# Optimization experiments

Hardware: AMD Instinct MI355X
Metric: run time of the kernel (lower is better)

Reference implementation:

```python
import jax, jax.numpy as jnp
import numpy as np

N, D, H = 2048, 128, 40


def setup_inputs() -> dict:
    key = jax.random.key(0)
    kx, kw, kv = jax.random.split(key, 3)
    X = jax.random.normal(kx, (N, D), dtype=jnp.float32)
    # nn.Parameter(torch.randn(D, D) / D) per head, stacked over H
    W = jax.random.normal(kw, (H, D, D), dtype=jnp.float32) / D
    V = jax.random.normal(kv, (H, D, D), dtype=jnp.float32) / D
    return {"X": X, "W": W, "V": V}


def reference(X, W, V):
    d = X.shape[1]
    # scores[h] = X @ W[h] @ X.T / sqrt(D)   -> [H, N, N]
    XW = jnp.einsum("nd,hde->hne", X, W)
    scores = jnp.einsum("hne,me->hnm", XW, X) / jnp.sqrt(jnp.asarray(d, X.dtype))
    # softmax over dim=1 of the 2D per-head score matrix == last axis here
    weights = jax.nn.softmax(scores, axis=-1) + 1e-8
    # A[h] = weights[h] @ X @ V[h]; output = sum over heads -> [N, D]
    XV = jnp.einsum("md,hde->hme", X, V)
    out = jnp.einsum("hnm,hme->ne", weights, XV)
    return out
```

## Files before the change

kernel.cpp:

```cpp
#include <hip/hip_runtime.h>
#include <hip/hip_bf16.h>
#include <stdint.h>

#define N 2048
#define D 128
#define H 40
#define NT 16

typedef __attribute__((ext_vector_type(8))) short short8;
typedef __attribute__((ext_vector_type(4))) float float4v;
typedef __attribute__((ext_vector_type(16))) float float16v;
typedef __attribute__((ext_vector_type(4))) _Float16 half4v;

static __device__ __forceinline__ unsigned short f32_to_bf16(float f) {
  unsigned int u = __builtin_bit_cast(unsigned int, f);
  unsigned int rounding = 0x7FFFu + ((u >> 16) & 1u);
  return (unsigned short)((u + rounding) >> 16);
}

static __device__ __forceinline__ unsigned int pk2(float lo, float hi) {
  return (unsigned int)f32_to_bf16(lo) | ((unsigned int)f32_to_bf16(hi) << 16);
}

static __device__ __forceinline__ unsigned int pk2f(float lo, float hi) {
  unsigned int a = __builtin_bit_cast(unsigned int, lo) + 0x8000u;
  unsigned int b = __builtin_bit_cast(unsigned int, hi) + 0x8000u;
  return __builtin_amdgcn_perm(b, a, 0x07060302u);
}

static __device__ __forceinline__ unsigned long long pack4(float x0, float x1,
                                                           float x2, float x3) {
  return (unsigned long long)pk2(x0, x1) | ((unsigned long long)pk2(x2, x3) << 32);
}

static __device__ __forceinline__ float fast_exp2(float x) {
#if __has_builtin(__builtin_amdgcn_exp2f)
  return __builtin_amdgcn_exp2f(x);
#else
  return __expf(0.69314718056f * x);
#endif
}

static __device__ __forceinline__ float bf2f(unsigned short u) {
  unsigned int x = ((unsigned int)u) << 16;
  return __builtin_bit_cast(float, x);
}

static __device__ __forceinline__ long long mk64(unsigned int lo, unsigned int hi) {
  return (long long)(((unsigned long long)hi << 32) | lo);
}

static __device__ __forceinline__ void load_lds16(const void* g, void* l) {
  __builtin_amdgcn_global_load_lds(
      (const __attribute__((address_space(1))) unsigned int*)g,
      (__attribute__((address_space(3))) unsigned int*)l, 16, 0, 0);
}

#define MFMA32(a, b, c) __builtin_amdgcn_mfma_f32_32x32x16_bf16((a), (b), (c), 0, 0, 0)
#define MFMA8(a, b, c) __builtin_amdgcn_mfma_f32_32x32x16_fp8_fp8((a), (b), (c), 0, 0, 0)

static __device__ __forceinline__ void regs_to_bfrags(const float16v c, int hh,
                                                      short8& f0, short8& f1) {
  unsigned int a0 = pk2f(c[0], c[1]),   a1 = pk2f(c[2], c[3]);
  unsigned int a2 = pk2f(c[4], c[5]),   a3 = pk2f(c[6], c[7]);
  unsigned int a4 = pk2f(c[8], c[9]),   a5 = pk2f(c[10], c[11]);
  unsigned int a6 = pk2f(c[12], c[13]), a7 = pk2f(c[14], c[15]);
  unsigned int x0 = __shfl_xor(hh ? a0 : a2, 32);
  unsigned int x1 = __shfl_xor(hh ? a1 : a3, 32);
  unsigned int x2 = __shfl_xor(hh ? a4 : a6, 32);
  unsigned int x3 = __shfl_xor(hh ? a5 : a7, 32);
  uint4 u0 = {hh ? x0 : a0, hh ? x1 : a1, hh ? a2 : x0, hh ? a3 : x1};
  uint4 u1 = {hh ? x2 : a4, hh ? x3 : a5, hh ? a6 : x2, hh ? a7 : x3};
  f0 = __builtin_bit_cast(short8, u0);
  f1 = __builtin_bit_cast(short8, u1);
}

static __device__ __forceinline__ void regs_to_f8frags(const float16v c, int hh,
                                                       long long& f0, long long& f1) {
  const float s = 64.0f;
  int v0 = __builtin_amdgcn_cvt_pk_fp8_f32(c[0] * s, c[1] * s, 0, false);
  v0 = __builtin_amdgcn_cvt_pk_fp8_f32(c[2] * s, c[3] * s, v0, true);
  int v1 = __builtin_amdgcn_cvt_pk_fp8_f32(c[4] * s, c[5] * s, 0, false);
  v1 = __builtin_amdgcn_cvt_pk_fp8_f32(c[6] * s, c[7] * s, v1, true);
  int v2 = __builtin_amdgcn_cvt_pk_fp8_f32(c[8] * s, c[9] * s, 0, false);
  v2 = __builtin_amdgcn_cvt_pk_fp8_f32(c[10] * s, c[11] * s, v2, true);
  int v3 = __builtin_amdgcn_cvt_pk_fp8_f32(c[12] * s, c[13] * s, 0, false);
  v3 = __builtin_amdgcn_cvt_pk_fp8_f32(c[14] * s, c[15] * s, v3, true);
  int t0 = __shfl_xor(hh ? v0 : v1, 32);
  int t1 = __shfl_xor(hh ? v2 : v3, 32);
  f0 = hh ? mk64((unsigned)t0, (unsigned)v1) : mk64((unsigned)v0, (unsigned)t0);
  f1 = hh ? mk64((unsigned)t1, (unsigned)v3) : mk64((unsigned)v2, (unsigned)t1);
}

static __device__ __forceinline__ void regs_to_pfrags(const float16v s, int hh,
                                                      float& lsum, short8& f0,
                                                      short8& f1) {
  float e[16];
  float acc = 0.0f;
#pragma unroll
  for (int i = 0; i < 16; i++) { e[i] = fast_exp2(s[i] * 0.015625f); acc += e[i]; }
  lsum += acc;
  unsigned int a0 = pk2f(e[0], e[1]),   a1 = pk2f(e[2], e[3]);
  unsigned int a2 = pk2f(e[4], e[5]),   a3 = pk2f(e[6], e[7]);
  unsigned int a4 = pk2f(e[8], e[9]),   a5 = pk2f(e[10], e[11]);
  unsigned int a6 = pk2f(e[12], e[13]), a7 = pk2f(e[14], e[15]);
  unsigned int x0 = __shfl_xor(hh ? a0 : a2, 32);
  unsigned int x1 = __shfl_xor(hh ? a1 : a3, 32);
  unsigned int x2 = __shfl_xor(hh ? a4 : a6, 32);
  unsigned int x3 = __shfl_xor(hh ? a5 : a7, 32);
  uint4 u0 = {hh ? x0 : a0, hh ? x1 : a1, hh ? a2 : x0, hh ? a3 : x1};
  uint4 u1 = {hh ? x2 : a4, hh ? x3 : a5, hh ? a6 : x2, hh ? a7 : x3};
  f0 = __builtin_bit_cast(short8, u0);
  f1 = __builtin_bit_cast(short8, u1);
}

static __device__ __forceinline__ void stage_64x256(const char* gbase, size_t stride,
                                                    int colOff, char* lds, int wave,
                                                    int lane) {
#pragma unroll
  for (int i = 0; i < 4; i++) {
    int r = wave * 16 + i * 4 + (lane >> 4);
    int us = (lane & 15) ^ (r & 15);
    load_lds16(gbase + (size_t)r * stride + colOff + us * 16,
               lds + (wave * 16 + i * 4) * 256);
  }
}
static __device__ __forceinline__ void stage_128x256(const char* gbase, size_t stride,
                                                     char* lds, int wave, int lane) {
#pragma unroll
  for (int i = 0; i < 8; i++) {
    int r = wave * 32 + i * 4 + (lane >> 4);
    int us = (lane & 15) ^ (r & 15);
    load_lds16(gbase + (size_t)r * stride + us * 16, lds + (wave * 32 + i * 4) * 256);
  }
}
static __device__ __forceinline__ void stage_128x128(const char* gbase, size_t stride,
                                                     int colOff, char* lds, int wave,
                                                     int lane) {
#pragma unroll
  for (int i = 0; i < 4; i++) {
    int m = wave * 16 + i * 4 + (lane >> 4);
    int u = (lane & 15) ^ (m & 15);
    int grow = 2 * m + (u >> 3);
    load_lds16(gbase + (size_t)grow * stride + colOff + (u & 7) * 16,
               lds + (wave * 16 + i * 4) * 256);
  }
}
static __device__ __forceinline__ void stage_k8(const char* gbase, char* lds,
                                                int wave, int lane) {
#pragma unroll
  for (int i = 0; i < 2; i++) {
    int m = wave * 8 + i * 4 + (lane >> 4);
    int u = (lane & 15) ^ (m & 15);
    int grow = 2 * m + (u >> 3);
    load_lds16(gbase + (size_t)grow * 128 + (u & 7) * 16,
               lds + (wave * 8 + i * 4) * 256);
  }
}
static __device__ __forceinline__ short8 read_macro(const char* lds, int row, int kunit) {
  int m = row >> 1;
  int u = ((row & 1) << 3) | kunit;
  return *(const short8*)(lds + m * 256 + ((u ^ (m & 15)) * 16));
}

__global__ __launch_bounds__(256)
void prep_kernel(const float* __restrict__ X, const float* __restrict__ W,
                 const float* __restrict__ V, unsigned short* __restrict__ Xb,
                 unsigned short* __restrict__ XbT, unsigned char* __restrict__ Xf8,
                 unsigned short* __restrict__ Wt, unsigned short* __restrict__ Vt) {
  const int tid = threadIdx.x;
  __shared__ __align__(16) unsigned short Lt[128 * 136];
  if (blockIdx.x < 16) {
    const int n0 = blockIdx.x * 128;
    for (int i = tid; i < 128 * 32; i += 256) {
      int row = i >> 5, c4 = (i & 31) * 4;
      float4v x = *(const float4v*)(X + (size_t)(n0 + row) * D + c4);
      unsigned long long p = pack4(x.x, x.y, x.z, x.w);
      *(unsigned long long*)(Lt + row * 136 + c4) = p;
      *(unsigned long long*)(Xb + (size_t)(n0 + row) * D + c4) = p;
    }
    __syncthreads();
    for (int i = tid; i < 128 * 16; i += 256) {
      int d = i >> 4, g = i & 15;
      short8 v;
#pragma unroll
      for (int j = 0; j < 8; j++) v[j] = (short)Lt[(g * 8 + j) * 136 + d];
      *(short8*)(XbT + (size_t)d * N + n0 + g * 8) = v;
    }
    for (int i = tid; i < 128 * 8; i += 256) {
      int row = i >> 3, c = i & 7, t = c >> 1, o8 = (c & 1) * 8;
      const unsigned short* lp = Lt + row * 136;
      int d0 = t * 32 + o8, d1 = t * 32 + 16 + o8;
      short8 xa = *(const short8*)(lp + d0);
      short8 xb = *(const short8*)(lp + d1);
      int w0 = __builtin_amdgcn_cvt_pk_fp8_f32(bf2f(xa[0]), bf2f(xa[1]), 0, false);
      w0 = __builtin_amdgcn_cvt_pk_fp8_f32(bf2f(xa[2]), bf2f(xa[3]), w0, true);
      int w1 = __builtin_amdgcn_cvt_pk_fp8_f32(bf2f(xa[4]), bf2f(xa[5]), 0, false);
      w1 = __builtin_amdgcn_cvt_pk_fp8_f32(bf2f(xa[6]), bf2f(xa[7]), w1, true);
      int w2 = __builtin_amdgcn_cvt_pk_fp8_f32(bf2f(xb[0]), bf2f(xb[1]), 0, false);
      w2 = __builtin_amdgcn_cvt_pk_fp8_f32(bf2f(xb[2]), bf2f(xb[3]), w2, true);
      int w3 = __builtin_amdgcn_cvt_pk_fp8_f32(bf2f(xb[4]), bf2f(xb[5]), 0, false);
      w3 = __builtin_amdgcn_cvt_pk_fp8_f32(bf2f(xb[6]), bf2f(xb[7]), w3, true);
      uint4 st = {(unsigned)w0, (unsigned)w1, (unsigned)w2, (unsigned)w3};
      *(uint4*)(Xf8 + (size_t)(n0 + row) * 128 + c * 16) = st;
    }
  } else {
    const int b = blockIdx.x - 16;
    const int mat = (b >= H) ? 1 : 0;
    const int h = mat ? b - H : b;
    const float* src = (mat ? V : W) + (size_t)h * D * D;
    unsigned short* dst = (mat ? Vt : Wt) + (size_t)h * D * D;
    const float scale = mat ? 1.0f : 0.1275174313f;
    for (int i = tid; i < 128 * 32; i += 256) {
      int d = i >> 5, e4 = (i & 31) * 4;
      float4v w = *(const float4v*)(src + d * D + e4);
      Lt[(e4 + 0) * 136 + d] = f32_to_bf16(w.x * scale);
      Lt[(e4 + 1) * 136 + d] = f32_to_bf16(w.y * scale);
      Lt[(e4 + 2) * 136 + d] = f32_to_bf16(w.z * scale);
      Lt[(e4 + 3) * 136 + d] = f32_to_bf16(w.w * scale);
    }
    __syncthreads();
    for (int i = tid; i < 128 * 16; i += 256) {
      int e = i >> 4, u = i & 15;
      *(uint4*)((char*)dst + (size_t)e * 256 + u * 16) =
          *(const uint4*)((const char*)Lt + (size_t)e * 272 + u * 16);
    }
  }
}

__global__ __launch_bounds__(256)
void attn_kernel(const unsigned short* __restrict__ Xb,
                 const unsigned char* __restrict__ Xf8,
                 const unsigned short* __restrict__ XbT,
                 const unsigned short* __restrict__ Wt,
                 const unsigned short* __restrict__ Vt,
                 unsigned short* __restrict__ Opart, float* __restrict__ Lsum) {
  __shared__ __align__(16) char smem[49152];
  char* XA = smem;
  char* XB = smem + 16384;
  char* KA = smem + 32768;
  char* KB = smem + 40960;
  const int bx = blockIdx.x;
  const int kh = bx & 1;
  const int q0 = ((bx >> 1) & 15) << 7;
  const int h = bx >> 5;
  const int tid = threadIdx.x;
  const int wave = tid >> 6, lane = tid & 63;
  const int l = lane & 31, hh = lane >> 5;

  const char* XbB = (const char*)Xb;
  const char* Xf8B = (const char*)Xf8;
  const char* XbTB = (const char*)XbT;
  const char* WtB = (const char*)(Wt + (size_t)h * D * D);
  const char* VtB = (const char*)(Vt + (size_t)h * D * D);
  const int kbase = kh * (N / 2);

  stage_128x256(WtB, 256, smem, wave, lane);
  stage_k8(Xf8B + (size_t)kbase * 128, KA, wave, lane);
  short8 xfr[8];
#pragma unroll
  for (int dk = 0; dk < 8; dk++)
    xfr[dk] = *(const short8*)(XbB + (size_t)(q0 + wave * 32 + l) * 256 + dk * 32 + hh * 16);
  __syncthreads();

  float16v qa[4];
#pragma unroll
  for (int et = 0; et < 4; et++) qa[et] = (float16v)0.0f;
#pragma unroll
  for (int et = 0; et < 4; et++) {
    const int r = et * 32 + l;
#pragma unroll
    for (int dk = 0; dk < 8; dk++) {
      short8 wa = *(const short8*)(smem + r * 256 + (((2 * dk + hh) ^ (r & 15)) * 16));
      qa[et] = MFMA32(wa, xfr[dk], qa[et]);
    }
  }
  long long qf8[8];
#pragma unroll
  for (int et = 0; et < 4; et++)
    regs_to_f8frags(qa[et], hh, qf8[2 * et], qf8[2 * et + 1]);

  float16v Tacc[4];
#pragma unroll
  for (int dt = 0; dt < 4; dt++) Tacc[dt] = (float16v)0.0f;
  float lsum = 0.0f;
  __syncthreads();

  stage_128x128(XbTB, 4096, kbase * 2, XA, wave, lane);
  __syncthreads();

  for (int kt = 0; kt < NT; kt++) {
    const char* curK = (kt & 1) ? KB : KA;
    const char* curX = (kt & 1) ? XB : XA;
    char* altK = (kt & 1) ? KA : KB;
    char* altX = (kt & 1) ? XA : XB;
    if (kt + 1 < NT) {
      const int k0n = kbase + (kt + 1) * 64;
      stage_k8(Xf8B + (size_t)k0n * 128, altK, wave, lane);
      stage_128x128(XbTB, 4096, k0n * 2, altX, wave, lane);
    } else {
      stage_64x256(VtB, 256, 0, altX, wave, lane);
    }
#pragma unroll
    for (int ksub = 0; ksub < 2; ksub++) {
      float16v s = (float16v)0.0f;
      const int krow = ksub * 32 + l;
      const int mb = (krow >> 1) * 256, m16 = (krow >> 1) & 15;
      const int rsel = (krow & 1) << 3;
#pragma unroll
      for (int t = 0; t < 4; t++) {
        int u = (rsel | (t * 2 + hh)) ^ m16;
        uint4 w = *(const uint4*)(curK + mb + u * 16);
        s = MFMA8(mk64(w.x, w.y), qf8[2 * t], s);
        s = MFMA8(mk64(w.z, w.w), qf8[2 * t + 1], s);
      }
      short8 pf0, pf1;
      regs_to_pfrags(s, hh, lsum, pf0, pf1);
#pragma unroll
      for (int kk = 0; kk < 2; kk++) {
        short8 pf = kk ? pf1 : pf0;
#pragma unroll
        for (int dt = 0; dt < 4; dt++) {
          short8 xt = read_macro(curX, dt * 32 + l, ksub * 4 + kk * 2 + hh);
          Tacc[dt] = MFMA32(xt, pf, Tacc[dt]);
        }
      }
    }
    __syncthreads();
  }

  float tot = lsum + __shfl_xor(lsum, 32);
  if (hh == 0) Lsum[(size_t)(h * 2 + kh) * N + q0 + wave * 32 + l] = tot;

  stage_64x256(VtB + 64 * 256, 256, 0, XB, wave, lane);
  short8 tb[8];
#pragma unroll
  for (int dt = 0; dt < 4; dt++)
    regs_to_bfrags(Tacc[dt], hh, tb[2 * dt], tb[2 * dt + 1]);

  float16v oacc[4];
#pragma unroll
  for (int et = 0; et < 4; et++) oacc[et] = (float16v)0.0f;
#pragma unroll
  for (int et = 0; et < 2; et++) {
    const int r = et * 32 + l;
#pragma unroll
    for (int dk = 0; dk < 8; dk++) {
      short8 va = *(const short8*)(XA + r * 256 + (((2 * dk + hh) ^ (r & 15)) * 16));
      oacc[et] = MFMA32(va, tb[dk], oacc[et]);
    }
  }
  __syncthreads();
#pragma unroll
  for (int et = 2; et < 4; et++) {
    const int r = (et - 2) * 32 + l;
#pragma unroll
    for (int dk = 0; dk < 8; dk++) {
      short8 va = *(const short8*)(XB + r * 256 + (((2 * dk + hh) ^ (r & 15)) * 16));
      oacc[et] = MFMA32(va, tb[dk], oacc[et]);
    }
  }

  unsigned short* Oph = Opart + (size_t)(h * 2 + kh) * N * D;
#pragma unroll
  for (int pass = 0; pass < 2; pass++) {
    __syncthreads();
    const int qrow = wave * 32 + l;
#pragma unroll
    for (int etL = 0; etL < 2; etL++) {
      int et = pass * 2 + etL;
#pragma unroll
      for (int g = 0; g < 4; g++) {
        int unit = etL * 8 + 2 * g + hh;
        float4v v;
        v.x = oacc[et][4 * g + 0];
        v.y = oacc[et][4 * g + 1];
        v.z = oacc[et][4 * g + 2];
        v.w = oacc[et][4 * g + 3];
        *(float4v*)(smem + qrow * 256 + ((unit ^ (qrow & 15)) * 16)) = v;
      }
    }
    __syncthreads();
#pragma unroll
    for (int i = 0; i < 8; i++) {
      int idx = i * 256 + tid;
      int qr = idx >> 4, up = idx & 15, u = up ^ (qr & 15);
      float4v v = *(const float4v*)(smem + qr * 256 + up * 16);
      auto h0 = __builtin_amdgcn_cvt_pkrtz(v.x, v.y);
      auto h1 = __builtin_amdgcn_cvt_pkrtz(v.z, v.w);
      uint2 st = {__builtin_bit_cast(unsigned int, h0),
                  __builtin_bit_cast(unsigned int, h1)};
      *(uint2*)(Oph + (size_t)(q0 + qr) * D + pass * 64 + u * 4) = st;
    }
  }
}

__global__ __launch_bounds__(256)
void reduce_kernel(const unsigned short* __restrict__ Opart,
                   const float* __restrict__ Lsum, float* __restrict__ out) {
  int idx = blockIdx.x * 256 + threadIdx.x;
  int n = idx >> 5;
  const uint2* base = (const uint2*)Opart;
  float4v acc = (float4v)0.0f;
#pragma unroll 8
  for (int h = 0; h < H; h++) {
    float lt = Lsum[(size_t)(2 * h) * N + n] + Lsum[(size_t)(2 * h + 1) * N + n];
    float il = __builtin_amdgcn_rcpf(lt);
    uint2 a = base[(size_t)(2 * h) * (N * D / 4) + idx];
    uint2 b = base[(size_t)(2 * h + 1) * (N * D / 4) + idx];
    float4v fa = __builtin_convertvector(__builtin_bit_cast(half4v, a), float4v);
    float4v fb = __builtin_convertvector(__builtin_bit_cast(half4v, b), float4v);
    acc += (fa + fb) * il;
  }
  *(float4v*)(out + (size_t)idx * 4) = acc;
}

extern "C" void kernel_launch(void* const* d_in, const int* in_sizes, int n_in,
                              void* d_out, int out_size, void* d_ws, size_t ws_size,
                              hipStream_t stream) {
  const float* X = (const float*)d_in[0];
  const float* W = (const float*)d_in[1];
  const float* V = (const float*)d_in[2];
  float* out = (float*)d_out;

  unsigned short* Xb = (unsigned short*)d_ws;
  unsigned short* XbT = Xb + (size_t)N * D;
  unsigned short* Wt = XbT + (size_t)N * D;
  unsigned short* Vt = Wt + (size_t)H * D * D;
  unsigned char* Xf8 = (unsigned char*)(Vt + (size_t)H * D * D);
  unsigned short* Opart = (unsigned short*)(Xf8 + (size_t)N * D);
  float* Lsum = (float*)(Opart + (size_t)H * 2 * N * D);

  prep_kernel<<<dim3(16 + 2 * H), 256, 0, stream>>>(X, W, V, Xb, XbT, Xf8, Wt, Vt);
  attn_kernel<<<dim3(NT * 2 * H), 256, 0, stream>>>(Xb, Xf8, XbT, Wt, Vt, Opart, Lsum);
  reduce_kernel<<<dim3(N * D / 4 / 256), 256, 0, stream>>>(Opart, Lsum, out);
}
```

Before: 191.3 us.

## Use 512-thread attention blocks over 256 query rows with shared K/V staging

The attention kernel now runs 8 waves per block, each block covering 256 query rows instead of 128, so each staged K/X/V tile in LDS is reused by twice as many query rows and the grid is halved. The staging helpers are rewritten so each wave loads a smaller share, and the output write-out is split into quarter passes. Prep uses more, smaller X blocks, and the reduce kernel processes two elements per thread with more threads. The cost is fewer blocks (640) for occupancy and more barrier phases in the epilogue.

```diff
diff --git a/kernel.cpp b/kernel.cpp
--- a/kernel.cpp
+++ b/kernel.cpp
@@ -8,9 +8,10 @@
 #define NT 16
 
 typedef __attribute__((ext_vector_type(8))) short short8;
+typedef __attribute__((ext_vector_type(2))) float float2v;
 typedef __attribute__((ext_vector_type(4))) float float4v;
 typedef __attribute__((ext_vector_type(16))) float float16v;
-typedef __attribute__((ext_vector_type(4))) _Float16 half4v;
+typedef __attribute__((ext_vector_type(2))) _Float16 half2v;
 
 static __device__ __forceinline__ unsigned short f32_to_bf16(float f) {
   unsigned int u = __builtin_bit_cast(unsigned int, f);
@@ -114,48 +115,42 @@
   f1 = __builtin_bit_cast(short8, u1);
 }
 
-static __device__ __forceinline__ void stage_64x256(const char* gbase, size_t stride,
-                                                    int colOff, char* lds, int wave,
-                                                    int lane) {
+static __device__ __forceinline__ void stage_64x256_w8(const char* gbase, size_t stride,
+                                                       char* lds, int wave, int lane) {
+#pragma unroll
+  for (int i = 0; i < 2; i++) {
+    int r = wave * 8 + i * 4 + (lane >> 4);
+    int us = (lane & 15) ^ (r & 15);
+    load_lds16(gbase + (size_t)r * stride + us * 16, lds + (wave * 8 + i * 4) * 256);
+  }
+}
+static __device__ __forceinline__ void stage_128x256_w8(const char* gbase, size_t stride,
+                                                        char* lds, int wave, int lane) {
 #pragma unroll
   for (int i = 0; i < 4; i++) {
     int r = wave * 16 + i * 4 + (lane >> 4);
     int us = (lane & 15) ^ (r & 15);
-    load_lds16(gbase + (size_t)r * stride + colOff + us * 16,
-               lds + (wave * 16 + i * 4) * 256);
-  }
-}
-static __device__ __forceinline__ void stage_128x256(const char* gbase, size_t stride,
-                                                     char* lds, int wave, int lane) {
-#pragma unroll
-  for (int i = 0; i < 8; i++) {
-    int r = wave * 32 + i * 4 + (lane >> 4);
-    int us = (lane & 15) ^ (r & 15);
-    load_lds16(gbase + (size_t)r * stride + us * 16, lds + (wave * 32 + i * 4) * 256);
-  }
-}
-static __device__ __forceinline__ void stage_128x128(const char* gbase, size_t stride,
-                                                     int colOff, char* lds, int wave,
-                                                     int lane) {
-#pragma unroll
-  for (int i = 0; i < 4; i++) {
-    int m = wave * 16 + i * 4 + (lane >> 4);
-    int u = (lane & 15) ^ (m & 15);
-    int grow = 2 * m + (u >> 3);
-    load_lds16(gbase + (size_t)grow * stride + colOff + (u & 7) * 16,
-               lds + (wave * 16 + i * 4) * 256);
-  }
-}
-static __device__ __forceinline__ void stage_k8(const char* gbase, char* lds,
-                                                int wave, int lane) {
+    load_lds16(gbase + (size_t)r * stride + us * 16, lds + (wave * 16 + i * 4) * 256);
+  }
+}
+static __device__ __forceinline__ void stage_128x128_w8(const char* gbase, size_t stride,
+                                                        int colOff, char* lds, int wave,
+                                                        int lane) {
 #pragma unroll
   for (int i = 0; i < 2; i++) {
     int m = wave * 8 + i * 4 + (lane >> 4);
     int u = (lane & 15) ^ (m & 15);
     int grow = 2 * m + (u >> 3);
-    load_lds16(gbase + (size_t)grow * 128 + (u & 7) * 16,
+    load_lds16(gbase + (size_t)grow * stride + colOff + (u & 7) * 16,
                lds + (wave * 8 + i * 4) * 256);
   }
+}
+static __device__ __forceinline__ void stage_k8_w8(const char* gbase, char* lds,
+                                                   int wave, int lane) {
+  int m = wave * 4 + (lane >> 4);
+  int u = (lane & 15) ^ (m & 15);
+  int grow = 2 * m + (u >> 3);
+  load_lds16(gbase + (size_t)grow * 128 + (u & 7) * 16, lds + (wave * 4) * 256);
 }
 static __device__ __forceinline__ short8 read_macro(const char* lds, int row, int kunit) {
   int m = row >> 1;
@@ -170,9 +165,9 @@
                  unsigned short* __restrict__ Wt, unsigned short* __restrict__ Vt) {
   const int tid = threadIdx.x;
   __shared__ __align__(16) unsigned short Lt[128 * 136];
-  if (blockIdx.x < 16) {
-    const int n0 = blockIdx.x * 128;
-    for (int i = tid; i < 128 * 32; i += 256) {
+  if (blockIdx.x < 32) {
+    const int n0 = blockIdx.x * 64;
+    for (int i = tid; i < 64 * 32; i += 256) {
       int row = i >> 5, c4 = (i & 31) * 4;
       float4v x = *(const float4v*)(X + (size_t)(n0 + row) * D + c4);
       unsigned long long p = pack4(x.x, x.y, x.z, x.w);
@@ -180,14 +175,14 @@
       *(unsigned long long*)(Xb + (size_t)(n0 + row) * D + c4) = p;
     }
     __syncthreads();
-    for (int i = tid; i < 128 * 16; i += 256) {
-      int d = i >> 4, g = i & 15;
+    for (int i = tid; i < 128 * 8; i += 256) {
+      int d = i >> 3, g = i & 7;
       short8 v;
 #pragma unroll
       for (int j = 0; j < 8; j++) v[j] = (short)Lt[(g * 8 + j) * 136 + d];
       *(short8*)(XbT + (size_t)d * N + n0 + g * 8) = v;
     }
-    for (int i = tid; i < 128 * 8; i += 256) {
+    for (int i = tid; i < 64 * 8; i += 256) {
       int row = i >> 3, c = i & 7, t = c >> 1, o8 = (c & 1) * 8;
       const unsigned short* lp = Lt + row * 136;
       int d0 = t * 32 + o8, d1 = t * 32 + 16 + o8;
@@ -205,7 +200,7 @@
       *(uint4*)(Xf8 + (size_t)(n0 + row) * 128 + c * 16) = st;
     }
   } else {
-    const int b = blockIdx.x - 16;
+    const int b = blockIdx.x - 32;
     const int mat = (b >= H) ? 1 : 0;
     const int h = mat ? b - H : b;
     const float* src = (mat ? V : W) + (size_t)h * D * D;
@@ -228,7 +223,7 @@
   }
 }
 
-__global__ __launch_bounds__(256)
+__global__ __launch_bounds__(512)
 void attn_kernel(const unsigned short* __restrict__ Xb,
                  const unsigned char* __restrict__ Xf8,
                  const unsigned short* __restrict__ XbT,
@@ -242,8 +237,8 @@
   char* KB = smem + 40960;
   const int bx = blockIdx.x;
   const int kh = bx & 1;
-  const int q0 = ((bx >> 1) & 15) << 7;
-  const int h = bx >> 5;
+  const int q0 = ((bx >> 1) & 7) << 8;
+  const int h = bx >> 4;
   const int tid = threadIdx.x;
   const int wave = tid >> 6, lane = tid & 63;
   const int l = lane & 31, hh = lane >> 5;
@@ -255,8 +250,8 @@
   const char* VtB = (const char*)(Vt + (size_t)h * D * D);
   const int kbase = kh * (N / 2);
 
-  stage_128x256(WtB, 256, smem, wave, lane);
-  stage_k8(Xf8B + (size_t)kbase * 128, KA, wave, lane);
+  stage_128x256_w8(WtB, 256, smem, wave, lane);
+  stage_k8_w8(Xf8B + (size_t)kbase * 128, KA, wave, lane);
   short8 xfr[8];
 #pragma unroll
   for (int dk = 0; dk < 8; dk++)
@@ -286,7 +281,7 @@
   float lsum = 0.0f;
   __syncthreads();
 
-  stage_128x128(XbTB, 4096, kbase * 2, XA, wave, lane);
+  stage_128x128_w8(XbTB, 4096, kbase * 2, XA, wave, lane);
   __syncthreads();
 
   for (int kt = 0; kt < NT; kt++) {
@@ -296,10 +291,10 @@
     char* altX = (kt & 1) ? XA : XB;
     if (kt + 1 < NT) {
       const int k0n = kbase + (kt + 1) * 64;
-      stage_k8(Xf8B + (size_t)k0n * 128, altK, wave, lane);
-      stage_128x128(XbTB, 4096, k0n * 2, altX, wave, lane);
+      stage_k8_w8(Xf8B + (size_t)k0n * 128, altK, wave, lane);
+      stage_128x128_w8(XbTB, 4096, k0n * 2, altX, wave, lane);
     } else {
-      stage_64x256(VtB, 256, 0, altX, wave, lane);
+      stage_64x256_w8(VtB, 256, altX, wave, lane);
     }
 #pragma unroll
     for (int ksub = 0; ksub < 2; ksub++) {
@@ -332,7 +327,7 @@
   float tot = lsum + __shfl_xor(lsum, 32);
   if (hh == 0) Lsum[(size_t)(h * 2 + kh) * N + q0 + wave * 32 + l] = tot;
 
-  stage_64x256(VtB + 64 * 256, 256, 0, XB, wave, lane);
+  stage_64x256_w8(VtB + 64 * 256, 256, XB, wave, lane);
   short8 tb[8];
 #pragma unroll
   for (int dt = 0; dt < 4; dt++)
@@ -363,56 +358,60 @@
 
   unsigned short* Oph = Opart + (size_t)(h * 2 + kh) * N * D;
 #pragma unroll
-  for (int pass = 0; pass < 2; pass++) {
-    __syncthreads();
-    const int qrow = wave * 32 + l;
-#pragma unroll
-    for (int etL = 0; etL < 2; etL++) {
-      int et = pass * 2 + etL;
-#pragma unroll
-      for (int g = 0; g < 4; g++) {
-        int unit = etL * 8 + 2 * g + hh;
-        float4v v;
-        v.x = oacc[et][4 * g + 0];
-        v.y = oacc[et][4 * g + 1];
-        v.z = oacc[et][4 * g + 2];
-        v.w = oacc[et][4 * g + 3];
-        *(float4v*)(smem + qrow * 256 + ((unit ^ (qrow & 15)) * 16)) = v;
+  for (int qh = 0; qh < 2; qh++)
+#pragma unroll
+    for (int eh = 0; eh < 2; eh++) {
+      __syncthreads();
+      if ((wave >> 2) == qh) {
+        const int qrow = (wave & 3) * 32 + l;
+#pragma unroll
+        for (int etL = 0; etL < 2; etL++) {
+          int et = eh * 2 + etL;
+#pragma unroll
+          for (int g = 0; g < 4; g++) {
+            int unit = etL * 8 + 2 * g + hh;
+            float4v v;
+            v.x = oacc[et][4 * g + 0];
+            v.y = oacc[et][4 * g + 1];
+            v.z = oacc[et][4 * g + 2];
+            v.w = oacc[et][4 * g + 3];
+            *(float4v*)(smem + qrow * 256 + ((unit ^ (qrow & 15)) * 16)) = v;
+          }
+        }
       }
-    }
-    __syncthreads();
-#pragma unroll
-    for (int i = 0; i < 8; i++) {
-      int idx = i * 256 + tid;
-      int qr = idx >> 4, up = idx & 15, u = up ^ (qr & 15);
-      float4v v = *(const float4v*)(smem + qr * 256 + up * 16);
-      auto h0 = __builtin_amdgcn_cvt_pkrtz(v.x, v.y);
-      auto h1 = __builtin_amdgcn_cvt_pkrtz(v.z, v.w);
-      uint2 st = {__builtin_bit_cast(unsigned int, h0),
-                  __builtin_bit_cast(unsigned int, h1)};
-      *(uint2*)(Oph + (size_t)(q0 + qr) * D + pass * 64 + u * 4) = st;
-    }
-  }
+      __syncthreads();
+#pragma unroll
+      for (int i = 0; i < 4; i++) {
+        int idx = i * 512 + tid;
+        int qr = idx >> 4, up = idx & 15, u = up ^ (qr & 15);
+        float4v v = *(const float4v*)(smem + qr * 256 + up * 16);
+        auto h0 = __builtin_amdgcn_cvt_pkrtz(v.x, v.y);
+        auto h1 = __builtin_amdgcn_cvt_pkrtz(v.z, v.w);
+        uint2 st = {__builtin_bit_cast(unsigned int, h0),
+                    __builtin_bit_cast(unsigned int, h1)};
+        *(uint2*)(Oph + (size_t)(q0 + qh * 128 + qr) * D + eh * 64 + u * 4) = st;
+      }
+    }
 }
 
 __global__ __launch_bounds__(256)
 void reduce_kernel(const unsigned short* __restrict__ Opart,
                    const float* __restrict__ Lsum, float* __restrict__ out) {
   int idx = blockIdx.x * 256 + threadIdx.x;
-  int n = idx >> 5;
-  const uint2* base = (const uint2*)Opart;
-  float4v acc = (float4v)0.0f;
+  int n = idx >> 6;
+  const unsigned int* base = (const unsigned int*)Opart;
+  float2v acc = (float2v)0.0f;
 #pragma unroll 8
   for (int h = 0; h < H; h++) {
     float lt = Lsum[(size_t)(2 * h) * N + n] + Lsum[(size_t)(2 * h + 1) * N + n];
     float il = __builtin_amdgcn_rcpf(lt);
-    uint2 a = base[(size_t)(2 * h) * (N * D / 4) + idx];
-    uint2 b = base[(size_t)(2 * h + 1) * (N * D / 4) + idx];
-    float4v fa = __builtin_convertvector(__builtin_bit_cast(half4v, a), float4v);
-    float4v fb = __builtin_convertvector(__builtin_bit_cast(half4v, b), float4v);
+    unsigned int a = base[(size_t)(2 * h) * (N * D / 2) + idx];
+    unsigned int b = base[(size_t)(2 * h + 1) * (N * D / 2) + idx];
+    float2v fa = __builtin_convertvector(__builtin_bit_cast(half2v, a), float2v);
+    float2v fb = __builtin_convertvector(__builtin_bit_cast(half2v, b), float2v);
     acc += (fa + fb) * il;
   }
-  *(float4v*)(out + (size_t)idx * 4) = acc;
+  *(float2v*)(out + (size_t)idx * 2) = acc;
 }
 
 extern "C" void kernel_launch(void* const* d_in, const int* in_sizes, int n_in,
@@ -431,7 +430,7 @@
   unsigned short* Opart = (unsigned short*)(Xf8 + (size_t)N * D);
   float* Lsum = (float*)(Opart + (size_t)H * 2 * N * D);
 
-  prep_kernel<<<dim3(16 + 2 * H), 256, 0, stream>>>(X, W, V, Xb, XbT, Xf8, Wt, Vt);
-  attn_kernel<<<dim3(NT * 2 * H), 256, 0, stream>>>(Xb, Xf8, XbT, Wt, Vt, Opart, Lsum);
-  reduce_kernel<<<dim3(N * D / 4 / 256), 256, 0, stream>>>(Opart, Lsum, out);
-}
+  prep_kernel<<<dim3(32 + 2 * H), 256, 0, stream>>>(X, W, V, Xb, XbT, Xf8, Wt, Vt);
+  attn_kernel<<<dim3(8 * 2 * H), 512, 0, stream>>>(Xb, Xf8, XbT, Wt, Vt, Opart, Lsum);
+  reduce_kernel<<<dim3(N * D / 2 / 256), 256, 0, stream>>>(Opart, Lsum, out);
+}
```

After: 200.3 us. +4.7%, slower.

## Precompute Q=X·W fp8 fragments in separate kernel; interleave two score tiles

Applied to the files above, without the earlier changes.

Moves the per-block Q projection (X·W[h]) out of the attention kernel into a new qprep kernel that writes fp8 fragments to workspace. The two key-split blocks no longer each recompute it, and the attention prologue drops the W staging and one barrier. The score loop is also restructured to compute both 32-row subtiles together, interleaving their MFMAs for more ILP. The cost is an extra kernel launch plus a global round-trip for Q, and higher register pressure from holding two score accumulators.

```diff
diff --git a/kernel.cpp b/kernel.cpp
--- a/kernel.cpp
+++ b/kernel.cpp
@@ -115,14 +115,12 @@
 }
 
 static __device__ __forceinline__ void stage_64x256(const char* gbase, size_t stride,
-                                                    int colOff, char* lds, int wave,
-                                                    int lane) {
+                                                    char* lds, int wave, int lane) {
 #pragma unroll
   for (int i = 0; i < 4; i++) {
     int r = wave * 16 + i * 4 + (lane >> 4);
     int us = (lane & 15) ^ (r & 15);
-    load_lds16(gbase + (size_t)r * stride + colOff + us * 16,
-               lds + (wave * 16 + i * 4) * 256);
+    load_lds16(gbase + (size_t)r * stride + us * 16, lds + (wave * 16 + i * 4) * 256);
   }
 }
 static __device__ __forceinline__ void stage_128x256(const char* gbase, size_t stride,
@@ -229,10 +227,54 @@
 }
 
 __global__ __launch_bounds__(256)
-void attn_kernel(const unsigned short* __restrict__ Xb,
+void qprep_kernel(const unsigned short* __restrict__ Xb,
+                  const unsigned short* __restrict__ Wt,
+                  unsigned char* __restrict__ Qf8g) {
+  __shared__ __align__(16) char smem[32768];
+  const int bx = blockIdx.x;
+  const int h = bx >> 4;
+  const int q0 = (bx & 15) << 7;
+  const int tid = threadIdx.x;
+  const int wave = tid >> 6, lane = tid & 63;
+  const int l = lane & 31, hh = lane >> 5;
+
+  stage_128x256((const char*)(Wt + (size_t)h * D * D), 256, smem, wave, lane);
+  short8 xfr[8];
+#pragma unroll
+  for (int dk = 0; dk < 8; dk++)
+    xfr[dk] = *(const short8*)((const char*)Xb +
+              (size_t)(q0 + wave * 32 + l) * 256 + dk * 32 + hh * 16);
+  __syncthreads();
+
+  float16v qa[4];
+#pragma unroll
+  for (int et = 0; et < 4; et++) qa[et] = (float16v)0.0f;
+#pragma unroll
+  for (int et = 0; et < 4; et++) {
+    const int r = et * 32 + l;
+#pragma unroll
+    for (int dk = 0; dk < 8; dk++) {
+      short8 wa = *(const short8*)(smem + r * 256 + (((2 * dk + hh) ^ (r & 15)) * 16));
+      qa[et] = MFMA32(wa, xfr[dk], qa[et]);
+    }
+  }
+  char* base = (char*)Qf8g + ((size_t)bx * 4 + wave) * 4096;
+#pragma unroll
+  for (int et = 0; et < 4; et++) {
+    long long f0, f1;
+    regs_to_f8frags(qa[et], hh, f0, f1);
+    uint4 st = {(unsigned)(unsigned long long)f0,
+                (unsigned)((unsigned long long)f0 >> 32),
+                (unsigned)(unsigned long long)f1,
+                (unsigned)((unsigned long long)f1 >> 32)};
+    *(uint4*)(base + et * 1024 + lane * 16) = st;
+  }
+}
+
+__global__ __launch_bounds__(256)
+void attn_kernel(const unsigned char* __restrict__ Qf8g,
                  const unsigned char* __restrict__ Xf8,
                  const unsigned short* __restrict__ XbT,
-                 const unsigned short* __restrict__ Wt,
                  const unsigned short* __restrict__ Vt,
                  unsigned short* __restrict__ Opart, float* __restrict__ Lsum) {
   __shared__ __align__(16) char smem[49152];
@@ -242,51 +284,34 @@
   char* KB = smem + 40960;
   const int bx = blockIdx.x;
   const int kh = bx & 1;
-  const int q0 = ((bx >> 1) & 15) << 7;
+  const int qt = (bx >> 1) & 15;
+  const int q0 = qt << 7;
   const int h = bx >> 5;
   const int tid = threadIdx.x;
   const int wave = tid >> 6, lane = tid & 63;
   const int l = lane & 31, hh = lane >> 5;
 
-  const char* XbB = (const char*)Xb;
   const char* Xf8B = (const char*)Xf8;
   const char* XbTB = (const char*)XbT;
-  const char* WtB = (const char*)(Wt + (size_t)h * D * D);
   const char* VtB = (const char*)(Vt + (size_t)h * D * D);
   const int kbase = kh * (N / 2);
 
-  stage_128x256(WtB, 256, smem, wave, lane);
   stage_k8(Xf8B + (size_t)kbase * 128, KA, wave, lane);
-  short8 xfr[8];
-#pragma unroll
-  for (int dk = 0; dk < 8; dk++)
-    xfr[dk] = *(const short8*)(XbB + (size_t)(q0 + wave * 32 + l) * 256 + dk * 32 + hh * 16);
-  __syncthreads();
-
-  float16v qa[4];
-#pragma unroll
-  for (int et = 0; et < 4; et++) qa[et] = (float16v)0.0f;
-#pragma unroll
-  for (int et = 0; et < 4; et++) {
-    const int r = et * 32 + l;
-#pragma unroll
-    for (int dk = 0; dk < 8; dk++) {
-      short8 wa = *(const short8*)(smem + r * 256 + (((2 * dk + hh) ^ (r & 15)) * 16));
-      qa[et] = MFMA32(wa, xfr[dk], qa[et]);
-    }
-  }
+  stage_128x128(XbTB, 4096, kbase * 2, XA, wave, lane);
   long long qf8[8];
-#pragma unroll
-  for (int et = 0; et < 4; et++)
-    regs_to_f8frags(qa[et], hh, qf8[2 * et], qf8[2 * et + 1]);
-
+  {
+    const char* qp = (const char*)Qf8g + (((size_t)h * 16 + qt) * 4 + wave) * 4096;
+#pragma unroll
+    for (int i = 0; i < 4; i++) {
+      uint4 v = *(const uint4*)(qp + i * 1024 + lane * 16);
+      qf8[2 * i] = mk64(v.x, v.y);
+      qf8[2 * i + 1] = mk64(v.z, v.w);
+    }
+  }
   float16v Tacc[4];
 #pragma unroll
   for (int dt = 0; dt < 4; dt++) Tacc[dt] = (float16v)0.0f;
   float lsum = 0.0f;
-  __syncthreads();
-
-  stage_128x128(XbTB, 4096, kbase * 2, XA, wave, lane);
   __syncthreads();
 
   for (int kt = 0; kt < NT; kt++) {
@@ -299,40 +324,43 @@
       stage_k8(Xf8B + (size_t)k0n * 128, altK, wave, lane);
       stage_128x128(XbTB, 4096, k0n * 2, altX, wave, lane);
     } else {
-      stage_64x256(VtB, 256, 0, altX, wave, lane);
-    }
-#pragma unroll
-    for (int ksub = 0; ksub < 2; ksub++) {
-      float16v s = (float16v)0.0f;
-      const int krow = ksub * 32 + l;
-      const int mb = (krow >> 1) * 256, m16 = (krow >> 1) & 15;
-      const int rsel = (krow & 1) << 3;
+      stage_64x256(VtB, 256, altX, wave, lane);
+    }
+    float16v s0 = (float16v)0.0f, s1 = (float16v)0.0f;
+    {
+      const int m0 = l >> 1, r0 = (l & 1) << 3;
+      const int m1 = (32 + l) >> 1, r1 = (l & 1) << 3;
 #pragma unroll
       for (int t = 0; t < 4; t++) {
-        int u = (rsel | (t * 2 + hh)) ^ m16;
-        uint4 w = *(const uint4*)(curK + mb + u * 16);
-        s = MFMA8(mk64(w.x, w.y), qf8[2 * t], s);
-        s = MFMA8(mk64(w.z, w.w), qf8[2 * t + 1], s);
+        int u0 = (r0 | (t * 2 + hh)) ^ (m0 & 15);
+        int u1 = (r1 | (t * 2 + hh)) ^ (m1 & 15);
+        uint4 w0 = *(const uint4*)(curK + m0 * 256 + u0 * 16);
+        uint4 w1 = *(const uint4*)(curK + m1 * 256 + u1 * 16);
+        s0 = MFMA8(mk64(w0.x, w0.y), qf8[2 * t], s0);
+        s1 = MFMA8(mk64(w1.x, w1.y), qf8[2 * t], s1);
+        s0 = MFMA8(mk64(w0.z, w0.w), qf8[2 * t + 1], s0);
+        s1 = MFMA8(mk64(w1.z, w1.w), qf8[2 * t + 1], s1);
       }
-      short8 pf0, pf1;
-      regs_to_pfrags(s, hh, lsum, pf0, pf1);
-#pragma unroll
-      for (int kk = 0; kk < 2; kk++) {
-        short8 pf = kk ? pf1 : pf0;
-#pragma unroll
-        for (int dt = 0; dt < 4; dt++) {
-          short8 xt = read_macro(curX, dt * 32 + l, ksub * 4 + kk * 2 + hh);
-          Tacc[dt] = MFMA32(xt, pf, Tacc[dt]);
-        }
+    }
+    short8 pf0[2], pf1[2];
+    regs_to_pfrags(s0, hh, lsum, pf0[0], pf0[1]);
+    regs_to_pfrags(s1, hh, lsum, pf1[0], pf1[1]);
+#pragma unroll
+    for (int kk = 0; kk < 2; kk++)
+#pragma unroll
+      for (int dt = 0; dt < 4; dt++) {
+        short8 xt0 = read_macro(curX, dt * 32 + l, kk * 2 + hh);
+        Tacc[dt] = MFMA32(xt0, pf0[kk], Tacc[dt]);
+        short8 xt1 = read_macro(curX, dt * 32 + l, 4 + kk * 2 + hh);
+        Tacc[dt] = MFMA32(xt1, pf1[kk], Tacc[dt]);
       }
-    }
     __syncthreads();
   }
 
   float tot = lsum + __shfl_xor(lsum, 32);
   if (hh == 0) Lsum[(size_t)(h * 2 + kh) * N + q0 + wave * 32 + l] = tot;
 
-  stage_64x256(VtB + 64 * 256, 256, 0, XB, wave, lane);
+  stage_64x256(VtB + 64 * 256, 256, XB, wave, lane);
   short8 tb[8];
 #pragma unroll
   for (int dt = 0; dt < 4; dt++)
@@ -428,10 +456,12 @@
   unsigned short* Wt = XbT + (size_t)N * D;
   unsigned short* Vt = Wt + (size_t)H * D * D;
   unsigned char* Xf8 = (unsigned char*)(Vt + (size_t)H * D * D);
-  unsigned short* Opart = (unsigned short*)(Xf8 + (size_t)N * D);
+  unsigned char* Qf8g = Xf8 + (size_t)N * D;
+  unsigned short* Opart = (unsigned short*)(Qf8g + (size_t)H * 16 * 4 * 4096);
   float* Lsum = (float*)(Opart + (size_t)H * 2 * N * D);
 
   prep_kernel<<<dim3(16 + 2 * H), 256, 0, stream>>>(X, W, V, Xb, XbT, Xf8, Wt, Vt);
-  attn_kernel<<<dim3(NT * 2 * H), 256, 0, stream>>>(Xb, Xf8, XbT, Wt, Vt, Opart, Lsum);
+  qprep_kernel<<<dim3(16 * H), 256, 0, stream>>>(Xb, Wt, Qf8g);
+  attn_kernel<<<dim3(NT * 2 * H), 256, 0, stream>>>(Qf8g, Xf8, XbT, Vt, Opart, Lsum);
   reduce_kernel<<<dim3(N * D / 4 / 256), 256, 0, stream>>>(Opart, Lsum, out);
 }
```

Result: slower. 196.2 us (+2.6%).
